# Kernel optimization log

Hardware: AMD Instinct MI355X
Metric: run time of the kernel (lower is better)

The kernel has to match this reference:

```python
import jax, jax.numpy as jnp
import numpy as np

B, C_IN, S = 64, 3, 16
N = S * S            # 256 oscillators
NUM_CN = 32
T_STEPS = 40
MAX_TIME = 5.0
DT = MAX_TIME / T_STEPS
TWO_PI = 6.283185307179586


def setup_inputs() -> dict:
    key = jax.random.key(0)
    ks = jax.random.split(key, 9)
    x = jax.random.normal(ks[0], (B, C_IN, S, S), jnp.float32)
    conv_w0 = jax.random.normal(ks[1], (16, C_IN, 3, 3), jnp.float32) * 0.1
    conv_b0 = jnp.zeros((16,), jnp.float32)
    conv_w1 = jax.random.normal(ks[2], (32, 16, 3, 3), jnp.float32) * 0.05
    conv_b1 = jnp.zeros((32,), jnp.float32)
    in_feat = 32 * N          # out_channels * img_side^2 = 8192
    out_feat = N * NUM_CN     # 8192
    lin_w = jax.random.normal(ks[3], (in_feat, out_feat), jnp.float32) * 0.01
    lin_b = jnp.zeros((out_feat,), jnp.float32)
    connectivity = jax.random.randint(ks[4], (N, NUM_CN), 0, N, dtype=jnp.int64)
    phase0 = jax.random.uniform(ks[5], (B, N), jnp.float32) * TWO_PI
    return {"x": x, "conv_w0": conv_w0, "conv_b0": conv_b0,
            "conv_w1": conv_w1, "conv_b1": conv_b1,
            "lin_w": lin_w, "lin_b": lin_b,
            "connectivity": connectivity, "phase0": phase0}


def _conv_tanh(x, w, b):
    y = jax.lax.conv_general_dilated(
        x, w, window_strides=(1, 1), padding="SAME",
        dimension_numbers=("NCHW", "OIHW", "NCHW"))
    return jnp.tanh(y + b[None, :, None, None])


def reference(x, conv_w0, conv_b0, conv_w1, conv_b1, lin_w, lin_b,
              connectivity, phase0):
    # conv stack with tanh (dropout in eval mode == identity)
    h = _conv_tanh(x, conv_w0, conv_b0)
    h = _conv_tanh(h, conv_w1, conv_b1)
    feat = h.reshape(h.shape[0], -1)                      # [B, 32*N]
    couplings = (feat @ lin_w + lin_b).reshape(-1, N, NUM_CN)
    couplings = couplings / jnp.linalg.norm(couplings, axis=2, keepdims=True)
    # scatter sparse couplings into dense [B, N, N] via connectivity indices
    rows = jnp.arange(N)[:, None]                         # [N, 1]
    K = jnp.zeros((couplings.shape[0], N, N), couplings.dtype)
    K = K.at[:, rows, connectivity].add(couplings)
    # n = number of nonzero couplings per row (abs(sign(K)).sum(2))
    n = jnp.sum(jnp.abs(jnp.sign(K)), axis=2)             # [B, N]
    # Euler integration of Kuramoto dynamics (ODEDynamic.forward per step)
    def step(phase, _):
        s, c = jnp.sin(phase), jnp.cos(phase)
        dphi = (jnp.einsum("bnm,bm->bn", K, s) * c
                - jnp.einsum("bnm,bm->bn", K, c) * s) / n
        phase_new = phase + DT * dphi
        return phase_new, phase_new
    _, phases = jax.lax.scan(step, phase0, None, length=T_STEPS)  # [T, B, N]
    return phases, K
```

## Files before the change

kernel.cpp:

```cpp
#include <hip/hip_runtime.h>

typedef __attribute__((ext_vector_type(8))) short short8;
typedef __attribute__((ext_vector_type(4))) float f32x4;
typedef unsigned short ushort_t;

#define N_OSC   256
#define NUM_CN  32
#define BATCH   64
#define T_STEPS 40
#define DT      0.125f

#define GK      8192
#define GN      8192
#define BN      64
#define KSPLIT  8
#define KRANGE  1024
#define BK      64
#define NCHUNK  16
#define PH_ELEMS 655360

__device__ __forceinline__ unsigned short f2bf(float f) {
    unsigned u = __float_as_uint(f);
    return (unsigned short)((u + 0x7fffu + ((u >> 16) & 1u)) >> 16);
}

__device__ __forceinline__ void stage16(const float* g, float* l) {
    __builtin_amdgcn_global_load_lds(
        (const __attribute__((address_space(1))) void*)g,
        (__attribute__((address_space(3))) void*)l, 16, 0, 0);
}

__global__ __launch_bounds__(256) void conv_kernel(
    const float* __restrict__ x,  const float* __restrict__ w0,
    const float* __restrict__ b0, const float* __restrict__ w1,
    const float* __restrict__ b1, ushort_t* __restrict__ featB)
{
    __shared__ float xs[3][256];
    __shared__ float h0[16][256];
    int blk = blockIdx.x;
    int b = blk >> 2, og = blk & 3;
    int p = threadIdx.x;
    int y = p >> 4, x0 = p & 15;

    #pragma unroll
    for (int c = 0; c < 3; ++c) xs[c][p] = x[b * 768 + c * 256 + p];
    __syncthreads();

    float acc0[16];
    #pragma unroll
    for (int o = 0; o < 16; ++o) acc0[o] = b0[o];
    #pragma unroll
    for (int c = 0; c < 3; ++c)
        #pragma unroll
        for (int ky = 0; ky < 3; ++ky) {
            int yy = y + ky - 1;
            if (yy < 0 || yy > 15) continue;
            #pragma unroll
            for (int kx = 0; kx < 3; ++kx) {
                int xx = x0 + kx - 1;
                if (xx < 0 || xx > 15) continue;
                float v = xs[c][yy * 16 + xx];
                #pragma unroll
                for (int o = 0; o < 16; ++o)
                    acc0[o] = fmaf(v, w0[o * 27 + c * 9 + ky * 3 + kx], acc0[o]);
            }
        }
    #pragma unroll
    for (int o = 0; o < 16; ++o) h0[o][p] = tanhf(acc0[o]);
    __syncthreads();

    float acc1[8];
    #pragma unroll
    for (int o = 0; o < 8; ++o) acc1[o] = b1[og * 8 + o];
    for (int c = 0; c < 16; ++c)
        #pragma unroll
        for (int ky = 0; ky < 3; ++ky) {
            int yy = y + ky - 1;
            if (yy < 0 || yy > 15) continue;
            #pragma unroll
            for (int kx = 0; kx < 3; ++kx) {
                int xx = x0 + kx - 1;
                if (xx < 0 || xx > 15) continue;
                float v = h0[c][yy * 16 + xx];
                #pragma unroll
                for (int o = 0; o < 8; ++o)
                    acc1[o] = fmaf(v, w1[(og * 8 + o) * 144 + c * 9 + ky * 3 + kx], acc1[o]);
            }
        }
    #pragma unroll
    for (int o = 0; o < 8; ++o)
        featB[b * 8192 + (og * 8 + o) * 256 + p] = f2bf(tanhf(acc1[o]));
}

__global__ __launch_bounds__(256, 4) void gemm_kernel(
    const ushort_t* __restrict__ featB,
    const float*    __restrict__ lin_w,
    float*          __restrict__ partials)
{
    __shared__ float ldsB[2][4096];
    int tid  = threadIdx.x;
    int lane = tid & 63, wid = tid >> 6;
    int l15  = lane & 15;
    int kg   = lane >> 4;
    int n0   = blockIdx.x * BN;
    int k0   = blockIdx.y * KRANGE;

    int st_kb = tid >> 4;
    int st_cp = (tid & 15) * 4;

    f32x4 acc[4];
    #pragma unroll
    for (int nf = 0; nf < 4; ++nf) acc[nf] = (f32x4){0.f, 0.f, 0.f, 0.f};

    const float* gb = lin_w + (size_t)k0 * GN + n0;

    #pragma unroll
    for (int i = 0; i < 4; ++i) {
        int k = i * 16 + st_kb;
        int c0 = st_cp ^ (((k >> 3) & 3) << 4);
        stage16(gb + (size_t)k * GN + c0, &ldsB[0][ i * 1024 + wid * 256 ]);
    }

    int arow = wid * 16 + l15;
    const ushort_t* abase = featB + (size_t)arow * GK + k0 + kg * 8;

    #pragma unroll 2
    for (int c = 0; c < NCHUNK; ++c) {
        int cur = c & 1;
        __syncthreads();
        if (c + 1 < NCHUNK) {
            const float* gn = gb + (size_t)(c + 1) * BK * GN;
            #pragma unroll
            for (int i = 0; i < 4; ++i) {
                int k = i * 16 + st_kb;
                int c0 = st_cp ^ (((k >> 3) & 3) << 4);
                stage16(gn + (size_t)k * GN + c0, &ldsB[cur ^ 1][ i * 1024 + wid * 256 ]);
            }
        }
        #pragma unroll
        for (int kk = 0; kk < 2; ++kk) {
            short8 af = *(const short8*)(abase + c * BK + kk * 32);
            #pragma unroll
            for (int nf = 0; nf < 4; ++nf) {
                int colswz = (nf * 16 + l15) ^ (kg << 4);
                const float* bsrc = &ldsB[cur][(kk * 32 + kg * 8) * 64 + colswz];
                short8 bfrag;
                #pragma unroll
                for (int i = 0; i < 8; ++i)
                    bfrag[i] = (short)f2bf(bsrc[i * 64]);
                acc[nf] = __builtin_amdgcn_mfma_f32_16x16x32_bf16(af, bfrag, acc[nf], 0, 0, 0);
            }
        }
    }

    float* pout = partials + (size_t)blockIdx.y * (64 * GN) + n0;
    int r4 = (lane >> 4) * 4;
    #pragma unroll
    for (int nf = 0; nf < 4; ++nf)
        #pragma unroll
        for (int r = 0; r < 4; ++r)
            pout[(size_t)(wid * 16 + r4 + r) * GN + nf * 16 + l15] = acc[nf][r];
}

__global__ __launch_bounds__(128) void reduce_norm_kernel(
    const float* __restrict__ partials, const float* __restrict__ lin_b,
    float* __restrict__ cpl)
{
    int idx = blockIdx.x * 128 + threadIdx.x;
    int b = idx >> 8, n = idx & 255;
    float c[32];
    const float* lb = lin_b + n * 32;
    #pragma unroll
    for (int k = 0; k < 32; ++k) c[k] = lb[k];
    const float* pp = partials + (size_t)b * GN + n * 32;
    #pragma unroll
    for (int y = 0; y < KSPLIT; ++y) {
        const float4* p4 = (const float4*)(pp + (size_t)y * (64 * GN));
        #pragma unroll
        for (int k4 = 0; k4 < 8; ++k4) {
            float4 v = p4[k4];
            c[k4 * 4 + 0] += v.x; c[k4 * 4 + 1] += v.y;
            c[k4 * 4 + 2] += v.z; c[k4 * 4 + 3] += v.w;
        }
    }
    float ss = 0.f;
    #pragma unroll
    for (int k = 0; k < 32; ++k) ss += c[k] * c[k];
    float inv = 1.0f / sqrtf(ss);
    float4* o4 = (float4*)(cpl + (size_t)idx * 32);
    #pragma unroll
    for (int k4 = 0; k4 < 8; ++k4) {
        float4 v;
        v.x = c[k4 * 4 + 0] * inv; v.y = c[k4 * 4 + 1] * inv;
        v.z = c[k4 * 4 + 2] * inv; v.w = c[k4 * 4 + 3] * inv;
        o4[k4] = v;
    }
}

__global__ __launch_bounds__(256) void scatter_kernel(
    const float* __restrict__ cpl, const int* __restrict__ conn,
    float* __restrict__ Kout, float* __restrict__ ncount)
{
    __shared__ float rows[4][256];
    int lane = threadIdx.x & 63, wid = threadIdx.x >> 6;
    int ridx = blockIdx.x * 4 + wid;
    int n = ridx & 255;

    #pragma unroll
    for (int i = 0; i < 4; ++i) rows[wid][lane * 4 + i] = 0.f;
    __syncthreads();
    if (lane < 32) {
        int j = conn[n * 32 + lane];
        float v = cpl[(size_t)ridx * 32 + lane];
        atomicAdd(&rows[wid][j], v);
    }
    __syncthreads();
    float4 vv = *(float4*)&rows[wid][lane * 4];
    int cnt = (vv.x != 0.f) + (vv.y != 0.f) + (vv.z != 0.f) + (vv.w != 0.f);
    #pragma unroll
    for (int off = 32; off; off >>= 1) cnt += __shfl_down(cnt, off);
    *(float4*)&Kout[(size_t)ridx * 256 + lane * 4] = vv;
    if (lane == 0) ncount[ridx] = (float)cnt;
}

__global__ __launch_bounds__(256) void ode_kernel(
    const float* __restrict__ cpl, const int* __restrict__ conn,
    const float* __restrict__ ncount, const float* __restrict__ phase0,
    float* __restrict__ phases)
{
    __shared__ float2 sc[256];
    int b = blockIdx.x, n = threadIdx.x;
    float w[32]; int j[32];
    #pragma unroll
    for (int k = 0; k < 32; ++k) {
        w[k] = cpl[(size_t)(b * 256 + n) * 32 + k];
        j[k] = conn[n * 32 + k];
    }
    float inv = 1.0f / ncount[b * 256 + n];
    float ph = phase0[b * 256 + n];
    float* out = phases + b * 256 + n;
    for (int t = 0; t < T_STEPS; ++t) {
        float s, c;
        __sincosf(ph, &s, &c);
        sc[n] = make_float2(s, c);
        __syncthreads();
        float aS = 0.f, aC = 0.f;
        #pragma unroll
        for (int k = 0; k < 32; ++k) {
            float2 v = sc[j[k]];
            aS = fmaf(w[k], v.x, aS);
            aC = fmaf(w[k], v.y, aC);
        }
        ph += DT * (aS * c - aC * s) * inv;
        out[t * (BATCH * N_OSC)] = ph;
        __syncthreads();
    }
}

extern "C" void kernel_launch(void* const* d_in, const int* in_sizes, int n_in,
                              void* d_out, int out_size, void* d_ws, size_t ws_size,
                              hipStream_t stream) {
    const float* x      = (const float*)d_in[0];
    const float* w0     = (const float*)d_in[1];
    const float* b0     = (const float*)d_in[2];
    const float* w1     = (const float*)d_in[3];
    const float* b1     = (const float*)d_in[4];
    const float* lin_w  = (const float*)d_in[5];
    const float* lin_b  = (const float*)d_in[6];
    const int*   conn   = (const int*)d_in[7];
    const float* phase0 = (const float*)d_in[8];

    float* out    = (float*)d_out;
    float* phases = out;
    float* Kout   = out + PH_ELEMS;

    char* ws = (char*)d_ws;
    ushort_t* featB    = (ushort_t*)ws;
    float*    cpl      = (float*)(ws + (1 << 20));
    float*    ncount   = (float*)(ws + (3 << 20));
    float*    partials = (float*)(ws + (4 << 20));

    conv_kernel<<<dim3(256), dim3(256), 0, stream>>>(x, w0, b0, w1, b1, featB);
    gemm_kernel<<<dim3(GN / BN, KSPLIT), dim3(256), 0, stream>>>(featB, lin_w, partials);
    reduce_norm_kernel<<<dim3(128), dim3(128), 0, stream>>>(partials, lin_b, cpl);
    scatter_kernel<<<dim3(4096), dim3(256), 0, stream>>>(cpl, conn, Kout, ncount);
    ode_kernel<<<dim3(64), dim3(256), 0, stream>>>(cpl, conn, ncount, phase0, phases);
}
```

Baseline: 125.1 us.

## Restage GEMM so each wave converts its own B columns once, A via LDS

The split-K GEMM now assigns each wave a 16-column slice of the fp32 weight tile and iterates over four 16-row fragments of the activations. Activations are staged into a swizzled LDS buffer with async global-to-LDS loads, double-buffered alongside the weights. This removes the fourfold redundant fp32-to-bf16 conversion and LDS reads of the weight tile across waves, at the cost of extra LDS traffic and capacity for the activation tile.

```diff
diff --git a/kernel.cpp b/kernel.cpp
--- a/kernel.cpp
+++ b/kernel.cpp
@@ -24,7 +24,7 @@
     return (unsigned short)((u + 0x7fffu + ((u >> 16) & 1u)) >> 16);
 }
 
-__device__ __forceinline__ void stage16(const float* g, float* l) {
+__device__ __forceinline__ void stage16(const void* g, void* l) {
     __builtin_amdgcn_global_load_lds(
         (const __attribute__((address_space(1))) void*)g,
         (__attribute__((address_space(3))) void*)l, 16, 0, 0);
@@ -92,12 +92,13 @@
         featB[b * 8192 + (og * 8 + o) * 256 + p] = f2bf(tanhf(acc1[o]));
 }
 
-__global__ __launch_bounds__(256, 4) void gemm_kernel(
+__global__ __launch_bounds__(256, 4) void gemm2_kernel(
     const ushort_t* __restrict__ featB,
     const float*    __restrict__ lin_w,
     float*          __restrict__ partials)
 {
-    __shared__ float ldsB[2][4096];
+    __shared__ float    ldsB[2][4096];
+    __shared__ ushort_t ldsA[2][4096];
     int tid  = threadIdx.x;
     int lane = tid & 63, wid = tid >> 6;
     int l15  = lane & 15;
@@ -107,12 +108,15 @@
 
     int st_kb = tid >> 4;
     int st_cp = (tid & 15) * 4;
+    int sa_r8 = tid >> 3;
+    int sa_s  = (tid & 7) ^ ((tid >> 3) & 7);
 
     f32x4 acc[4];
     #pragma unroll
-    for (int nf = 0; nf < 4; ++nf) acc[nf] = (f32x4){0.f, 0.f, 0.f, 0.f};
+    for (int mf = 0; mf < 4; ++mf) acc[mf] = (f32x4){0.f, 0.f, 0.f, 0.f};
 
     const float* gb = lin_w + (size_t)k0 * GN + n0;
+    const ushort_t* ga = featB + k0;
 
     #pragma unroll
     for (int i = 0; i < 4; ++i) {
@@ -120,9 +124,11 @@
         int c0 = st_cp ^ (((k >> 3) & 3) << 4);
         stage16(gb + (size_t)k * GN + c0, &ldsB[0][ i * 1024 + wid * 256 ]);
     }
-
-    int arow = wid * 16 + l15;
-    const ushort_t* abase = featB + (size_t)arow * GK + k0 + kg * 8;
+    #pragma unroll
+    for (int i = 0; i < 2; ++i) {
+        int r = i * 32 + sa_r8;
+        stage16(ga + (size_t)r * GK + sa_s * 8, &ldsA[0][ i * 2048 + wid * 512 ]);
+    }
 
     #pragma unroll 2
     for (int c = 0; c < NCHUNK; ++c) {
@@ -130,36 +136,43 @@
         __syncthreads();
         if (c + 1 < NCHUNK) {
             const float* gn = gb + (size_t)(c + 1) * BK * GN;
+            const ushort_t* gan = ga + (c + 1) * BK;
             #pragma unroll
             for (int i = 0; i < 4; ++i) {
                 int k = i * 16 + st_kb;
                 int c0 = st_cp ^ (((k >> 3) & 3) << 4);
                 stage16(gn + (size_t)k * GN + c0, &ldsB[cur ^ 1][ i * 1024 + wid * 256 ]);
             }
+            #pragma unroll
+            for (int i = 0; i < 2; ++i) {
+                int r = i * 32 + sa_r8;
+                stage16(gan + (size_t)r * GK + sa_s * 8, &ldsA[cur ^ 1][ i * 2048 + wid * 512 ]);
+            }
         }
         #pragma unroll
         for (int kk = 0; kk < 2; ++kk) {
-            short8 af = *(const short8*)(abase + c * BK + kk * 32);
-            #pragma unroll
-            for (int nf = 0; nf < 4; ++nf) {
-                int colswz = (nf * 16 + l15) ^ (kg << 4);
-                const float* bsrc = &ldsB[cur][(kk * 32 + kg * 8) * 64 + colswz];
-                short8 bfrag;
-                #pragma unroll
-                for (int i = 0; i < 8; ++i)
-                    bfrag[i] = (short)f2bf(bsrc[i * 64]);
-                acc[nf] = __builtin_amdgcn_mfma_f32_16x16x32_bf16(af, bfrag, acc[nf], 0, 0, 0);
+            int colswz = (wid * 16 + l15) ^ (kg << 4);
+            const float* bsrc = &ldsB[cur][(kk * 32 + kg * 8) * 64 + colswz];
+            short8 bfrag;
+            #pragma unroll
+            for (int i = 0; i < 8; ++i)
+                bfrag[i] = (short)f2bf(bsrc[i * 64]);
+            #pragma unroll
+            for (int mf = 0; mf < 4; ++mf) {
+                int r = mf * 16 + l15;
+                int t = (kk * 4 + kg) ^ (r & 7);
+                short8 af = *(const short8*)&ldsA[cur][r * 64 + t * 8];
+                acc[mf] = __builtin_amdgcn_mfma_f32_16x16x32_bf16(af, bfrag, acc[mf], 0, 0, 0);
             }
         }
     }
 
     float* pout = partials + (size_t)blockIdx.y * (64 * GN) + n0;
-    int r4 = (lane >> 4) * 4;
-    #pragma unroll
-    for (int nf = 0; nf < 4; ++nf)
+    #pragma unroll
+    for (int mf = 0; mf < 4; ++mf)
         #pragma unroll
         for (int r = 0; r < 4; ++r)
-            pout[(size_t)(wid * 16 + r4 + r) * GN + nf * 16 + l15] = acc[nf][r];
+            pout[(size_t)(mf * 16 + kg * 4 + r) * GN + wid * 16 + l15] = acc[mf][r];
 }
 
 __global__ __launch_bounds__(128) void reduce_norm_kernel(
@@ -281,7 +294,7 @@
     float*    partials = (float*)(ws + (4 << 20));
 
     conv_kernel<<<dim3(256), dim3(256), 0, stream>>>(x, w0, b0, w1, b1, featB);
-    gemm_kernel<<<dim3(GN / BN, KSPLIT), dim3(256), 0, stream>>>(featB, lin_w, partials);
+    gemm2_kernel<<<dim3(GN / BN, KSPLIT), dim3(256), 0, stream>>>(featB, lin_w, partials);
     reduce_norm_kernel<<<dim3(128), dim3(128), 0, stream>>>(partials, lin_b, cpl);
     scatter_kernel<<<dim3(4096), dim3(256), 0, stream>>>(cpl, conn, Kout, ncount);
     ode_kernel<<<dim3(64), dim3(256), 0, stream>>>(cpl, conn, ncount, phase0, phases);
```

New measurement: 131.3 us. +5.0%, slower.

## Fuse split-K reduction, coupling scatter and ODE integration into one tail kernel

Applied to the files above, without the earlier changes.

Replaces the separate reduce_norm, scatter and ode kernels with a single per-batch tail kernel. Each block reduces the split-K partials and normalises its couplings into LDS, then scatters them row by row into the dense K output and counts nonzeros. It then runs the Euler loop using the couplings and counts held on chip. This removes two launches and the global round trips of the cpl and ncount buffers. In exchange, the 16 MB K write and the partials read are now handled by only 64 blocks, and the scatter runs 64 serial iterations with block-wide barriers, which may underuse the GPU.

```diff
diff --git a/kernel.cpp b/kernel.cpp
--- a/kernel.cpp
+++ b/kernel.cpp
@@ -24,7 +24,7 @@
     return (unsigned short)((u + 0x7fffu + ((u >> 16) & 1u)) >> 16);
 }
 
-__device__ __forceinline__ void stage16(const float* g, float* l) {
+__device__ __forceinline__ void stage16(const void* g, void* l) {
     __builtin_amdgcn_global_load_lds(
         (const __attribute__((address_space(1))) void*)g,
         (__attribute__((address_space(3))) void*)l, 16, 0, 0);
@@ -162,81 +162,67 @@
             pout[(size_t)(wid * 16 + r4 + r) * GN + nf * 16 + l15] = acc[nf][r];
 }
 
-__global__ __launch_bounds__(128) void reduce_norm_kernel(
+__global__ __launch_bounds__(256) void tail_kernel(
     const float* __restrict__ partials, const float* __restrict__ lin_b,
-    float* __restrict__ cpl)
+    const int* __restrict__ conn, const float* __restrict__ phase0,
+    float* __restrict__ Kout, float* __restrict__ phases)
 {
-    int idx = blockIdx.x * 128 + threadIdx.x;
-    int b = idx >> 8, n = idx & 255;
-    float c[32];
-    const float* lb = lin_b + n * 32;
-    #pragma unroll
-    for (int k = 0; k < 32; ++k) c[k] = lb[k];
-    const float* pp = partials + (size_t)b * GN + n * 32;
-    #pragma unroll
-    for (int y = 0; y < KSPLIT; ++y) {
-        const float4* p4 = (const float4*)(pp + (size_t)y * (64 * GN));
-        #pragma unroll
-        for (int k4 = 0; k4 < 8; ++k4) {
-            float4 v = p4[k4];
-            c[k4 * 4 + 0] += v.x; c[k4 * 4 + 1] += v.y;
-            c[k4 * 4 + 2] += v.z; c[k4 * 4 + 3] += v.w;
-        }
-    }
-    float ss = 0.f;
-    #pragma unroll
-    for (int k = 0; k < 32; ++k) ss += c[k] * c[k];
-    float inv = 1.0f / sqrtf(ss);
-    float4* o4 = (float4*)(cpl + (size_t)idx * 32);
-    #pragma unroll
-    for (int k4 = 0; k4 < 8; ++k4) {
-        float4 v;
-        v.x = c[k4 * 4 + 0] * inv; v.y = c[k4 * 4 + 1] * inv;
-        v.z = c[k4 * 4 + 2] * inv; v.w = c[k4 * 4 + 3] * inv;
-        o4[k4] = v;
-    }
-}
-
-__global__ __launch_bounds__(256) void scatter_kernel(
-    const float* __restrict__ cpl, const int* __restrict__ conn,
-    float* __restrict__ Kout, float* __restrict__ ncount)
-{
-    __shared__ float rows[4][256];
-    int lane = threadIdx.x & 63, wid = threadIdx.x >> 6;
-    int ridx = blockIdx.x * 4 + wid;
-    int n = ridx & 255;
-
-    #pragma unroll
-    for (int i = 0; i < 4; ++i) rows[wid][lane * 4 + i] = 0.f;
-    __syncthreads();
-    if (lane < 32) {
-        int j = conn[n * 32 + lane];
-        float v = cpl[(size_t)ridx * 32 + lane];
-        atomicAdd(&rows[wid][j], v);
-    }
-    __syncthreads();
-    float4 vv = *(float4*)&rows[wid][lane * 4];
-    int cnt = (vv.x != 0.f) + (vv.y != 0.f) + (vv.z != 0.f) + (vv.w != 0.f);
-    #pragma unroll
-    for (int off = 32; off; off >>= 1) cnt += __shfl_down(cnt, off);
-    *(float4*)&Kout[(size_t)ridx * 256 + lane * 4] = vv;
-    if (lane == 0) ncount[ridx] = (float)cnt;
-}
-
-__global__ __launch_bounds__(256) void ode_kernel(
-    const float* __restrict__ cpl, const int* __restrict__ conn,
-    const float* __restrict__ ncount, const float* __restrict__ phase0,
-    float* __restrict__ phases)
-{
+    __shared__ float  cplS[256][33];
+    __shared__ float  rows[4][256];
+    __shared__ float  ncountS[256];
     __shared__ float2 sc[256];
     int b = blockIdx.x, n = threadIdx.x;
-    float w[32]; int j[32];
-    #pragma unroll
-    for (int k = 0; k < 32; ++k) {
-        w[k] = cpl[(size_t)(b * 256 + n) * 32 + k];
-        j[k] = conn[n * 32 + k];
-    }
-    float inv = 1.0f / ncount[b * 256 + n];
+    int lane = n & 63, wid = n >> 6;
+
+    float w[32];
+    {
+        float c[32];
+        const float* lb = lin_b + n * 32;
+        #pragma unroll
+        for (int k = 0; k < 32; ++k) c[k] = lb[k];
+        const float* pp = partials + (size_t)b * GN + n * 32;
+        #pragma unroll
+        for (int y = 0; y < KSPLIT; ++y) {
+            const float4* p4 = (const float4*)(pp + (size_t)y * (64 * GN));
+            #pragma unroll
+            for (int k4 = 0; k4 < 8; ++k4) {
+                float4 v = p4[k4];
+                c[k4 * 4 + 0] += v.x; c[k4 * 4 + 1] += v.y;
+                c[k4 * 4 + 2] += v.z; c[k4 * 4 + 3] += v.w;
+            }
+        }
+        float ss = 0.f;
+        #pragma unroll
+        for (int k = 0; k < 32; ++k) ss += c[k] * c[k];
+        float inv = 1.0f / sqrtf(ss);
+        #pragma unroll
+        for (int k = 0; k < 32; ++k) {
+            w[k] = c[k] * inv;
+            cplS[n][k] = w[k];
+        }
+    }
+    __syncthreads();
+
+    for (int i = 0; i < 64; ++i) {
+        int row = wid * 64 + i;
+        *(float4*)&rows[wid][lane * 4] = (float4){0.f, 0.f, 0.f, 0.f};
+        __syncthreads();
+        if (lane < 32)
+            atomicAdd(&rows[wid][conn[row * 32 + lane]], cplS[row][lane]);
+        __syncthreads();
+        float4 vv = *(float4*)&rows[wid][lane * 4];
+        int cnt = (vv.x != 0.f) + (vv.y != 0.f) + (vv.z != 0.f) + (vv.w != 0.f);
+        #pragma unroll
+        for (int off = 32; off; off >>= 1) cnt += __shfl_down(cnt, off);
+        *(float4*)&Kout[((size_t)(b * 256 + row)) * 256 + lane * 4] = vv;
+        if (lane == 0) ncountS[row] = (float)cnt;
+    }
+    __syncthreads();
+
+    int j[32];
+    #pragma unroll
+    for (int k = 0; k < 32; ++k) j[k] = conn[n * 32 + k];
+    float inv = 1.0f / ncountS[n];
     float ph = phase0[b * 256 + n];
     float* out = phases + b * 256 + n;
     for (int t = 0; t < T_STEPS; ++t) {
@@ -276,13 +262,10 @@
 
     char* ws = (char*)d_ws;
     ushort_t* featB    = (ushort_t*)ws;
-    float*    cpl      = (float*)(ws + (1 << 20));
-    float*    ncount   = (float*)(ws + (3 << 20));
     float*    partials = (float*)(ws + (4 << 20));
 
     conv_kernel<<<dim3(256), dim3(256), 0, stream>>>(x, w0, b0, w1, b1, featB);
     gemm_kernel<<<dim3(GN / BN, KSPLIT), dim3(256), 0, stream>>>(featB, lin_w, partials);
-    reduce_norm_kernel<<<dim3(128), dim3(128), 0, stream>>>(partials, lin_b, cpl);
-    scatter_kernel<<<dim3(4096), dim3(256), 0, stream>>>(cpl, conn, Kout, ncount);
-    ode_kernel<<<dim3(64), dim3(256), 0, stream>>>(cpl, conn, ncount, phase0, phases);
-}
+    tail_kernel<<<dim3(64), dim3(256), 0, stream>>>(partials, lin_b, conn,
+                                                    phase0, Kout, phases);
+}
```

Result: slower. 163.8 us (+30.9%).
